# Optimization experiments

Measured on AMD Instinct MI355X. Metric: run time of the kernel, lower is better.

## Reference

```python
import jax, jax.numpy as jnp
import numpy as np

N = 16        # n_var
L = 16        # max_lags
H = 16        # hidden_dim
B = 32768     # batch
G = N * N     # n_var^2 groups


def setup_inputs() -> dict:
    key = jax.random.key(0)
    ks = jax.random.split(key, 8)
    x = jax.random.normal(ks[0], (B, G, L), dtype=jnp.float32)
    causal = jax.random.randint(ks[1], (N, N, L), 0, 2, dtype=jnp.int32)
    # torch Conv1d init: U(-sqrt(k), sqrt(k)), k = 1/(in_channels_per_group*kernel)
    s1 = 1.0 / np.sqrt(L)        # conv1: in/group=1, kernel=L
    s2 = 1.0 / np.sqrt(H)        # conv2: in/group=H, kernel=1
    s3 = 1.0 / np.sqrt(N * H)    # conv3: in/group=N*H, kernel=1
    W1 = jax.random.uniform(ks[2], (G, H, L), jnp.float32, -s1, s1)
    b1 = jax.random.uniform(ks[3], (G, H), jnp.float32, -s1, s1)
    W2 = jax.random.uniform(ks[4], (G, H, H), jnp.float32, -s2, s2)
    b2 = jax.random.uniform(ks[5], (G, H), jnp.float32, -s2, s2)
    W3 = jax.random.uniform(ks[6], (N, N * H), jnp.float32, -s3, s3)
    b3 = jax.random.uniform(ks[7], (N,), jnp.float32, -s3, s3)
    return {"x": x, "causal": causal, "W1": W1, "b1": b1,
            "W2": W2, "b2": b2, "W3": W3, "b3": b3}


def reference(x, causal, W1, b1, W2, b2, W3, b3):
    # mask = ~causal_matrix.bool() -> masked_fill with 0 == multiply by causal!=0
    mask = (causal != 0).reshape(1, G, L).astype(x.dtype)
    xm = x * mask                                          # [B, G, L]
    # conv1: per-group (1 -> H) over the full lag window (output length 1)
    h1 = jax.nn.sigmoid(jnp.einsum('bgl,ghl->bgh', xm, W1) + b1)   # [B, G, H]
    # conv2: per-group (H -> H) 1x1; W2[g, out, in]
    h2 = jax.nn.sigmoid(jnp.einsum('bgh,gkh->bgk', h1, W2) + b2)   # [B, G, H]
    # conv3: groups = n_var, per variable (N*H -> 1) 1x1
    h2f = h2.reshape(-1, N, N * H)                          # [B, N, N*H]
    out = jnp.einsum('bvm,vm->bv', h2f, W3) + b3            # [B, N]
    return out
```

## Files before the change

kernel.cpp:

```cpp
#include <hip/hip_runtime.h>
#include <hip/hip_bf16.h>

#define N_VAR 16
#define LAGS  16
#define HID   16
#define GRP   256
#define BATCH 32768
#define WPAD  20

typedef __attribute__((ext_vector_type(8))) short  bf16x8;
typedef __attribute__((ext_vector_type(4))) short  short4v;
typedef __attribute__((ext_vector_type(4))) float  floatx4;

__device__ __forceinline__ float sigmoid_fast(float t) {
    float e = __expf(-t);
    return __builtin_amdgcn_rcpf(1.0f + e);
}

__device__ __forceinline__ short f2bf(float f) {
    __hip_bfloat16 h = __float2bfloat16(f);
    return __builtin_bit_cast(short, h);
}

__global__ __launch_bounds__(256) void prep_weights(
    const float* __restrict__ W1, const float* __restrict__ W2,
    const int* __restrict__ causal,
    short* __restrict__ W1b, short* __restrict__ W2b)
{
    const int i = blockIdx.x * 256 + threadIdx.x;
    const int g = i >> 8;
    const int l = i & 15;
    const float msk = (causal[g * LAGS + l] != 0) ? 1.0f : 0.0f;
    W1b[i] = f2bf(W1[i] * msk);
    W2b[i] = f2bf(W2[i]);
}

__global__ __launch_bounds__(256) void additive_mfma(
    const float* __restrict__ x,
    const float* __restrict__ b1,
    const float* __restrict__ b2,
    const float* __restrict__ W3,
    const float* __restrict__ b3,
    const short* __restrict__ W1b,
    const short* __restrict__ W2b,
    float* __restrict__ out)
{
    __shared__ short w1s[16][16][WPAD];
    __shared__ short w2s[16][16][WPAD];
    __shared__ float b1s[16][16];
    __shared__ float b2s[16][16];
    __shared__ float w3s[16][16];

    const int t    = threadIdx.x;
    const int v    = blockIdx.x & (N_VAR - 1);
    const int bb   = blockIdx.x >> 4;
    const int widx = t >> 6;
    const int lane = t & 63;
    const int m    = lane & 15;
    const int q    = lane >> 4;
    const int b0   = bb * 64 + widx * 16;

    {
        const int n  = t >> 4;
        const int hh = t & 15;
        const short* s1 = W1b + (((v * N_VAR + n) * HID) + hh) * LAGS;
        const short* s2 = W2b + (((v * N_VAR + n) * HID) + hh) * HID;
        #pragma unroll
        for (int j = 0; j < 4; ++j) {
            *reinterpret_cast<short4v*>(&w1s[n][hh][j * 4]) =
                *reinterpret_cast<const short4v*>(s1 + j * 4);
            *reinterpret_cast<short4v*>(&w2s[n][hh][j * 4]) =
                *reinterpret_cast<const short4v*>(s2 + j * 4);
        }
        (&b1s[0][0])[t] = b1[v * GRP + t];
        (&b2s[0][0])[t] = b2[v * GRP + t];
        (&w3s[0][0])[t] = W3[v * (N_VAR * HID) + t];
    }
    __syncthreads();

    const float* __restrict__ xp =
        x + (size_t)(b0 + m) * (GRP * LAGS) + v * (N_VAR * LAGS) + q * 4;
    const float b3v = b3[v];
    float acc = 0.0f;

    const short* w1p = &w1s[0][m][q * 4];
    const short* w2p = &w2s[0][m][q * 4];
    const float* b1p = &b1s[0][q * 4];
    const float* b2p = &b2s[0][q * 4];
    const float* w3p = &w3s[0][q * 4];

    auto process = [&](int n, floatx4 xv) {
        const short4v w1v = *reinterpret_cast<const short4v*>(w1p + n * (16 * WPAD));
        bf16x8 fa1 = {w1v[0], w1v[1], w1v[2], w1v[3],
                      (short)0, (short)0, (short)0, (short)0};
        bf16x8 fx  = {f2bf(xv[0]), f2bf(xv[1]), f2bf(xv[2]), f2bf(xv[3]),
                      (short)0, (short)0, (short)0, (short)0};
        floatx4 c1 = *reinterpret_cast<const floatx4*>(b1p + n * 16);
        floatx4 d1 = __builtin_amdgcn_mfma_f32_16x16x32_bf16(fa1, fx, c1, 0, 0, 0);

        bf16x8 fb2 = {f2bf(sigmoid_fast(d1[0])), f2bf(sigmoid_fast(d1[1])),
                      f2bf(sigmoid_fast(d1[2])), f2bf(sigmoid_fast(d1[3])),
                      (short)0, (short)0, (short)0, (short)0};
        const short4v w2v = *reinterpret_cast<const short4v*>(w2p + n * (16 * WPAD));
        bf16x8 fa2 = {w2v[0], w2v[1], w2v[2], w2v[3],
                      (short)0, (short)0, (short)0, (short)0};
        floatx4 c2 = *reinterpret_cast<const floatx4*>(b2p + n * 16);
        floatx4 d2 = __builtin_amdgcn_mfma_f32_16x16x32_bf16(fa2, fb2, c2, 0, 0, 0);

        const floatx4 w3v = *reinterpret_cast<const floatx4*>(w3p + n * 16);
        acc += sigmoid_fast(d2[0]) * w3v[0];
        acc += sigmoid_fast(d2[1]) * w3v[1];
        acc += sigmoid_fast(d2[2]) * w3v[2];
        acc += sigmoid_fast(d2[3]) * w3v[3];
    };

    floatx4 cur0 = *reinterpret_cast<const floatx4*>(xp);
    floatx4 cur1 = *reinterpret_cast<const floatx4*>(xp + LAGS);

    #pragma unroll 1
    for (int np = 0; np < 8; ++np) {
        floatx4 nxt0, nxt1;
        if (np < 7) {
            nxt0 = *reinterpret_cast<const floatx4*>(xp + (2 * np + 2) * LAGS);
            nxt1 = *reinterpret_cast<const floatx4*>(xp + (2 * np + 3) * LAGS);
        }
        process(2 * np,     cur0);
        process(2 * np + 1, cur1);
        if (np < 7) { cur0 = nxt0; cur1 = nxt1; }
    }

    acc += __shfl_xor(acc, 16);
    acc += __shfl_xor(acc, 32);
    if (lane < 16)
        out[(size_t)(b0 + lane) * N_VAR + v] = acc + b3v;
}

extern "C" void kernel_launch(void* const* d_in, const int* in_sizes, int n_in,
                              void* d_out, int out_size, void* d_ws, size_t ws_size,
                              hipStream_t stream) {
    const float* x      = (const float*)d_in[0];
    const int*   causal = (const int*)  d_in[1];
    const float* W1     = (const float*)d_in[2];
    const float* b1     = (const float*)d_in[3];
    const float* W2     = (const float*)d_in[4];
    const float* b2     = (const float*)d_in[5];
    const float* W3     = (const float*)d_in[6];
    const float* b3     = (const float*)d_in[7];
    float* out          = (float*)d_out;

    short* W1b = (short*)d_ws;
    short* W2b = (short*)d_ws + GRP * HID * LAGS;

    prep_weights<<<(GRP * HID * LAGS) / 256, 256, 0, stream>>>(
        W1, W2, causal, W1b, W2b);

    const int n_blocks = (BATCH / 64) * N_VAR;
    additive_mfma<<<n_blocks, 256, 0, stream>>>(
        x, b1, b2, W3, b3, W1b, W2b, out);
}
```

Baseline: 693.7 us.

## Stage x tiles through swizzled LDS as bf16 with coalesced cooperative loads

Rather than each lane issuing strided 16-byte loads of x directly into registers, the block now cooperatively loads 64 rows × 8 groups × 16 lags per half in a coalesced pattern. It converts the values to bf16 and stores them in a swizzled LDS buffer, which the MFMA loop then reads. This targets poor global-memory coalescing, since the old per-lane reads were scattered. The cost is extra LDS traffic, two barriers per half, and the loss of the explicit prefetch overlap. Launch bounds also now request 4 blocks per CU.

```diff
diff --git a/kernel.cpp b/kernel.cpp
--- a/kernel.cpp
+++ b/kernel.cpp
@@ -35,7 +35,7 @@
     W2b[i] = f2bf(W2[i]);
 }
 
-__global__ __launch_bounds__(256) void additive_mfma(
+__global__ __launch_bounds__(256, 4) void additive_mfma(
     const float* __restrict__ x,
     const float* __restrict__ b1,
     const float* __restrict__ b2,
@@ -45,6 +45,7 @@
     const short* __restrict__ W2b,
     float* __restrict__ out)
 {
+    __shared__ short xs[64 * 128];
     __shared__ short w1s[16][16][WPAD];
     __shared__ short w2s[16][16][WPAD];
     __shared__ float b1s[16][16];
@@ -58,7 +59,8 @@
     const int lane = t & 63;
     const int m    = lane & 15;
     const int q    = lane >> 4;
-    const int b0   = bb * 64 + widx * 16;
+    const int row  = (widx << 4) + m;
+    const int b0   = (bb << 6) + (widx << 4);
 
     {
         const int n  = t >> 4;
@@ -76,10 +78,7 @@
         (&b2s[0][0])[t] = b2[v * GRP + t];
         (&w3s[0][0])[t] = W3[v * (N_VAR * HID) + t];
     }
-    __syncthreads();
 
-    const float* __restrict__ xp =
-        x + (size_t)(b0 + m) * (GRP * LAGS) + v * (N_VAR * LAGS) + q * 4;
     const float b3v = b3[v];
     float acc = 0.0f;
 
@@ -89,44 +88,56 @@
     const float* b2p = &b2s[0][q * 4];
     const float* w3p = &w3s[0][q * 4];
 
-    auto process = [&](int n, floatx4 xv) {
-        const short4v w1v = *reinterpret_cast<const short4v*>(w1p + n * (16 * WPAD));
-        bf16x8 fa1 = {w1v[0], w1v[1], w1v[2], w1v[3],
-                      (short)0, (short)0, (short)0, (short)0};
-        bf16x8 fx  = {f2bf(xv[0]), f2bf(xv[1]), f2bf(xv[2]), f2bf(xv[3]),
-                      (short)0, (short)0, (short)0, (short)0};
-        floatx4 c1 = *reinterpret_cast<const floatx4*>(b1p + n * 16);
-        floatx4 d1 = __builtin_amdgcn_mfma_f32_16x16x32_bf16(fa1, fx, c1, 0, 0, 0);
+    const float* __restrict__ xgbase =
+        x + (size_t)(bb * 64) * (GRP * LAGS) + v * (N_VAR * LAGS);
 
-        bf16x8 fb2 = {f2bf(sigmoid_fast(d1[0])), f2bf(sigmoid_fast(d1[1])),
-                      f2bf(sigmoid_fast(d1[2])), f2bf(sigmoid_fast(d1[3])),
-                      (short)0, (short)0, (short)0, (short)0};
-        const short4v w2v = *reinterpret_cast<const short4v*>(w2p + n * (16 * WPAD));
-        bf16x8 fa2 = {w2v[0], w2v[1], w2v[2], w2v[3],
-                      (short)0, (short)0, (short)0, (short)0};
-        floatx4 c2 = *reinterpret_cast<const floatx4*>(b2p + n * 16);
-        floatx4 d2 = __builtin_amdgcn_mfma_f32_16x16x32_bf16(fa2, fb2, c2, 0, 0, 0);
+    for (int half = 0; half < 2; ++half) {
+        #pragma unroll
+        for (int p = 0; p < 8; ++p) {
+            const int u = (p << 8) + t;
+            const int i = u >> 5;
+            const int c = u & 31;
+            const floatx4 f = *reinterpret_cast<const floatx4*>(
+                xgbase + (size_t)i * (GRP * LAGS) + (half * 8) * LAGS + c * 4);
+            short4v s = {f2bf(f[0]), f2bf(f[1]), f2bf(f[2]), f2bf(f[3])};
+            *reinterpret_cast<short4v*>(
+                &xs[(i << 7) + (((c + (i << 2)) & 31) << 2)]) = s;
+        }
+        __syncthreads();
 
-        const floatx4 w3v = *reinterpret_cast<const floatx4*>(w3p + n * 16);
-        acc += sigmoid_fast(d2[0]) * w3v[0];
-        acc += sigmoid_fast(d2[1]) * w3v[1];
-        acc += sigmoid_fast(d2[2]) * w3v[2];
-        acc += sigmoid_fast(d2[3]) * w3v[3];
-    };
+        #pragma unroll 2
+        for (int nl = 0; nl < 8; ++nl) {
+            const int n = (half << 3) + nl;
 
-    floatx4 cur0 = *reinterpret_cast<const floatx4*>(xp);
-    floatx4 cur1 = *reinterpret_cast<const floatx4*>(xp + LAGS);
+            const short4v xv = *reinterpret_cast<const short4v*>(
+                &xs[(row << 7) + ((((nl << 2) + q + (row << 2)) & 31) << 2)]);
+            bf16x8 fx = {xv[0], xv[1], xv[2], xv[3],
+                         (short)0, (short)0, (short)0, (short)0};
 
-    #pragma unroll 1
-    for (int np = 0; np < 8; ++np) {
-        floatx4 nxt0, nxt1;
-        if (np < 7) {
-            nxt0 = *reinterpret_cast<const floatx4*>(xp + (2 * np + 2) * LAGS);
-            nxt1 = *reinterpret_cast<const floatx4*>(xp + (2 * np + 3) * LAGS);
+            const short4v w1v = *reinterpret_cast<const short4v*>(
+                w1p + n * (16 * WPAD));
+            bf16x8 fa1 = {w1v[0], w1v[1], w1v[2], w1v[3],
+                          (short)0, (short)0, (short)0, (short)0};
+            floatx4 c1 = *reinterpret_cast<const floatx4*>(b1p + n * 16);
+            floatx4 d1 = __builtin_amdgcn_mfma_f32_16x16x32_bf16(fa1, fx, c1, 0, 0, 0);
+
+            bf16x8 fb2 = {f2bf(sigmoid_fast(d1[0])), f2bf(sigmoid_fast(d1[1])),
+                          f2bf(sigmoid_fast(d1[2])), f2bf(sigmoid_fast(d1[3])),
+                          (short)0, (short)0, (short)0, (short)0};
+            const short4v w2v = *reinterpret_cast<const short4v*>(
+                w2p + n * (16 * WPAD));
+            bf16x8 fa2 = {w2v[0], w2v[1], w2v[2], w2v[3],
+                          (short)0, (short)0, (short)0, (short)0};
+            floatx4 c2 = *reinterpret_cast<const floatx4*>(b2p + n * 16);
+            floatx4 d2 = __builtin_amdgcn_mfma_f32_16x16x32_bf16(fa2, fb2, c2, 0, 0, 0);
+
+            const floatx4 w3v = *reinterpret_cast<const floatx4*>(w3p + n * 16);
+            acc += sigmoid_fast(d2[0]) * w3v[0];
+            acc += sigmoid_fast(d2[1]) * w3v[1];
+            acc += sigmoid_fast(d2[2]) * w3v[2];
+            acc += sigmoid_fast(d2[3]) * w3v[3];
         }
-        process(2 * np,     cur0);
-        process(2 * np + 1, cur1);
-        if (np < 7) { cur0 = nxt0; cur1 = nxt1; }
+        __syncthreads();
     }
 
     acc += __shfl_xor(acc, 16);
```

New measurement: 677.1 us. 2.4% less time.
